# Optimization experiments

Measured on AMD Instinct MI355X. Metric: run time of the kernel, lower is better.

Reference implementation:

```python
import jax, jax.numpy as jnp
import numpy as np

NUM_MEMORIES = 4096
HIDDEN_DIM = 64
TEMPERATURE = 0.5
SHRINK_THRES = 0.0025
EPS = 1e-12


def _l2_normalize(v, axis=-1):
    # matches torch F.normalize: v / max(||v||_2, eps)
    n = jnp.sqrt(jnp.sum(v * v, axis=axis, keepdims=True))
    return v / jnp.maximum(n, EPS)


def _hard_shrink_relu(w, lambd):
    # relu(w - lambd) * w / (|w - lambd| + eps)
    d = w - lambd
    return jax.nn.relu(d) * w / (jnp.abs(d) + EPS)


def setup_inputs() -> dict:
    key = jax.random.key(0)
    kx, km = jax.random.split(key)
    x = jax.random.normal(kx, (16, 2048, HIDDEN_DIM), dtype=jnp.float32)
    # xavier_uniform for (num_memories, hidden_dim)
    bound = float(np.sqrt(6.0 / (NUM_MEMORIES + HIDDEN_DIM)))
    memories = jax.random.uniform(km, (NUM_MEMORIES, HIDDEN_DIM), dtype=jnp.float32,
                                  minval=-bound, maxval=bound)
    return {"x": x, "memories": memories}


def reference(x, memories):
    # cosine similarity addressing
    x_n = _l2_normalize(x, axis=-1)                      # [B,S,D]
    m_n = _l2_normalize(memories, axis=-1)               # [M,D]
    logits = jnp.einsum('bsd,md->bsm', x_n, m_n)         # [B,S,M]
    weight = jax.nn.softmax(logits / TEMPERATURE, axis=-1)
    # hard-shrink sparsification + L1 renormalization
    weight = _hard_shrink_relu(weight, SHRINK_THRES)
    l1 = jnp.sum(jnp.abs(weight), axis=-1, keepdims=True)
    weight = weight / jnp.maximum(l1, EPS)
    read = jnp.einsum('bsm,md->bsd', weight, memories)   # [B,S,D]
    return read, weight
```

## Files before the change

kernel.cpp:

```cpp
#include <hip/hip_runtime.h>
#include <hip/hip_bf16.h>


#define NM 4096
#define HD 64
#define NROWS 32768

typedef short bf16x8 __attribute__((ext_vector_type(8)));
typedef float f32x4  __attribute__((ext_vector_type(4)));

__global__ __launch_bounds__(256) void prep_rows(const float* __restrict__ src,
                                                 ushort* __restrict__ dst,
                                                 float scale) {
    const int wave = threadIdx.x >> 6, lane = threadIdx.x & 63;
    const long row = (long)blockIdx.x * 4 + wave;
    float v = src[row * HD + lane];
    float s = v * v;
#pragma unroll
    for (int o = 32; o; o >>= 1) s += __shfl_xor(s, o, 64);
    const float inv = scale / fmaxf(sqrtf(s), 1e-12f);
    __hip_bfloat16 h = __float2bfloat16(v * inv);
    dst[row * HD + lane] = *reinterpret_cast<ushort*>(&h);
}

__global__ __launch_bounds__(256) void prep_m_swz(const float* __restrict__ mem,
                                                  ushort* __restrict__ mbs) {
    const int wave = threadIdx.x >> 6, lane = threadIdx.x & 63;
    const int row = blockIdx.x * 4 + wave;
    float v = mem[row * HD + lane];
    float s = v * v;
#pragma unroll
    for (int o = 32; o; o >>= 1) s += __shfl_xor(s, o, 64);
    const float inv = 1.0f / fmaxf(sqrtf(s), 1e-12f);
    __hip_bfloat16 h = __float2bfloat16(v * inv);
    const int t = row >> 4, c = row & 15;
    const int k = lane;
    const int f = k >> 5, q = (k >> 3) & 3, j = k & 7;
    mbs[(long)t * 1024 + f * 512 + (q * 16 + c) * 8 + j] =
        *reinterpret_cast<ushort*>(&h);
}

__global__ __launch_bounds__(512, 4) void k_ps(const ushort* __restrict__ xb,
                                               const ushort* __restrict__ mbs,
                                               const float* __restrict__ mem,
                                               float* __restrict__ out_w,
                                               float* __restrict__ out_read) {
    const int tid = threadIdx.x;
    const int wv = tid >> 6, lane = tid & 63;
    const int m0 = blockIdx.x * 16;

    __shared__ float sS[4][16];
    __shared__ float sL[4][16];
    __shared__ uint  sD[4];
    __shared__ float sred[4][16][64];

    const float4 z4 = make_float4(0.0f, 0.0f, 0.0f, 0.0f);

    if (wv >= 4) {
        const int sw = wv - 4;
        float4* base = (float4*)(out_w + (long)m0 * NM);
#pragma unroll 8
        for (int it = 0; it < 64; it++)
            base[it * 256 + sw * 64 + lane] = z4;
        if (sw == 0) {
            float4* rb = (float4*)(out_read + (long)m0 * HD);
#pragma unroll
            for (int it = 0; it < 4; it++) rb[it * 64 + lane] = z4;
        }
        __syncthreads();
        __syncthreads();
        const uint anyd = sD[0] | sD[1] | sD[2] | sD[3];
        if (anyd) {
            __syncthreads();
            __syncthreads();
        }
        return;
    }

    const int q = lane >> 4, c = lane & 15;
    const int nbase = wv * 1024;
    const bf16x8 a0 = *(const bf16x8*)(xb + (long)(m0 + c) * HD + q * 8);
    const bf16x8 a1 = *(const bf16x8*)(xb + (long)(m0 + c) * HD + q * 8 + 32);
    const ushort* mstrip = mbs + (long)(wv * 64) * 1024;

    float tmax8[8];
    float sm[4] = {0.0f, 0.0f, 0.0f, 0.0f};
    for (int g = 0; g < 8; g++) {
        float tm = -1e30f;
#pragma unroll 4
        for (int ii = 0; ii < 8; ii++) {
            const int i = g * 8 + ii;
            const ushort* mc = mstrip + (long)i * 1024 + lane * 8;
            const bf16x8 b0 = *(const bf16x8*)(mc);
            const bf16x8 b1 = *(const bf16x8*)(mc + 512);
            f32x4 t = {0.0f, 0.0f, 0.0f, 0.0f};
            t = __builtin_amdgcn_mfma_f32_16x16x32_bf16(a0, b0, t, 0, 0, 0);
            t = __builtin_amdgcn_mfma_f32_16x16x32_bf16(a1, b1, t, 0, 0, 0);
            tm = fmaxf(tm, fmaxf(fmaxf(t[0], t[1]), fmaxf(t[2], t[3])));
#pragma unroll
            for (int r = 0; r < 4; r++) sm[r] += __expf(t[r]);
        }
        tmax8[g] = tm;
    }
#pragma unroll
    for (int o = 1; o < 16; o <<= 1)
#pragma unroll
        for (int r = 0; r < 4; r++) sm[r] += __shfl_xor(sm[r], o, 64);
    if (c == 0)
#pragma unroll
        for (int r = 0; r < 4; r++) sS[wv][q * 4 + r] = sm[r];
    __syncthreads();
    float rS[4], tmin = 1e30f;
#pragma unroll
    for (int r = 0; r < 4; r++) {
        const float S = sS[0][q * 4 + r] + sS[1][q * 4 + r] +
                        sS[2][q * 4 + r] + sS[3][q * 4 + r];
        rS[r] = 1.0f / S;
        const float tau = __logf(0.0025f * S) - 1e-3f;
        tmin = fminf(tmin, tau);
    }
    uint dmask = 0;
#pragma unroll
    for (int g = 0; g < 8; g++)
        if (__ballot(tmax8[g] > tmin)) dmask |= 1u << g;
    if (lane == 0) sD[wv] = dmask;
    __syncthreads();
    const uint anyd = sD[0] | sD[1] | sD[2] | sD[3];

    if (!anyd) return;

    float l1[4] = {0.0f, 0.0f, 0.0f, 0.0f};
    for (int g = 0; g < 8; g++) {
        if (!((dmask >> g) & 1u)) continue;
        for (int ii = 0; ii < 8; ii++) {
            const int i = g * 8 + ii;
            const ushort* mc = mstrip + (long)i * 1024 + lane * 8;
            const bf16x8 b0 = *(const bf16x8*)(mc);
            const bf16x8 b1 = *(const bf16x8*)(mc + 512);
            f32x4 t = {0.0f, 0.0f, 0.0f, 0.0f};
            t = __builtin_amdgcn_mfma_f32_16x16x32_bf16(a0, b0, t, 0, 0, 0);
            t = __builtin_amdgcn_mfma_f32_16x16x32_bf16(a1, b1, t, 0, 0, 0);
#pragma unroll
            for (int r = 0; r < 4; r++) {
                float w = __expf(t[r]) * rS[r];
                float d = w - 0.0025f;
                l1[r] += __fdividef(fmaxf(d, 0.0f) * w, fabsf(d) + 1e-12f);
            }
        }
    }
#pragma unroll
    for (int o = 1; o < 16; o <<= 1)
#pragma unroll
        for (int r = 0; r < 4; r++) l1[r] += __shfl_xor(l1[r], o, 64);
    if (c == 0)
#pragma unroll
        for (int r = 0; r < 4; r++) sL[wv][q * 4 + r] = l1[r];
    __syncthreads();
    float rL[4];
#pragma unroll
    for (int r = 0; r < 4; r++)
        rL[r] = 1.0f / fmaxf(sL[0][q * 4 + r] + sL[1][q * 4 + r] +
                             sL[2][q * 4 + r] + sL[3][q * 4 + r], 1e-12f);

    float racc[16];
#pragma unroll
    for (int r = 0; r < 16; r++) racc[r] = 0.0f;
    float* wbase = out_w + (long)(m0 + q * 4) * NM + c;
    for (int i = 0; i < 64; i++) {
        const int n0 = nbase + i * 16;
        const ushort* mc = mstrip + (long)i * 1024 + lane * 8;
        const bf16x8 b0 = *(const bf16x8*)(mc);
        const bf16x8 b1 = *(const bf16x8*)(mc + 512);
        f32x4 t = {0.0f, 0.0f, 0.0f, 0.0f};
        t = __builtin_amdgcn_mfma_f32_16x16x32_bf16(a0, b0, t, 0, 0, 0);
        t = __builtin_amdgcn_mfma_f32_16x16x32_bf16(a1, b1, t, 0, 0, 0);
        float wf[4];
#pragma unroll
        for (int r = 0; r < 4; r++) {
            float w  = __expf(t[r]) * rS[r];
            float d  = w - 0.0025f;
            float sh = __fdividef(fmaxf(d, 0.0f) * w, fabsf(d) + 1e-12f);
            wf[r] = sh * rL[r];
            wbase[(long)r * NM + n0] = wf[r];
        }
        const bool nz = (wf[0] != 0.0f) | (wf[1] != 0.0f) |
                        (wf[2] != 0.0f) | (wf[3] != 0.0f);
        unsigned long long mask = __ballot(nz);
        while (mask) {
            const int j = __ffsll((long long)mask) - 1;
            mask &= (mask - 1);
            const int qj = j >> 4, cj = j & 15;
            float b0v = __shfl(wf[0], j, 64), b1v = __shfl(wf[1], j, 64);
            float b2v = __shfl(wf[2], j, 64), b3v = __shfl(wf[3], j, 64);
            const float mv = mem[(long)(n0 + cj) * HD + lane];
            switch (qj) {
                case 0: racc[0]  += b0v * mv; racc[1]  += b1v * mv;
                        racc[2]  += b2v * mv; racc[3]  += b3v * mv; break;
                case 1: racc[4]  += b0v * mv; racc[5]  += b1v * mv;
                        racc[6]  += b2v * mv; racc[7]  += b3v * mv; break;
                case 2: racc[8]  += b0v * mv; racc[9]  += b1v * mv;
                        racc[10] += b2v * mv; racc[11] += b3v * mv; break;
                default: racc[12] += b0v * mv; racc[13] += b1v * mv;
                         racc[14] += b2v * mv; racc[15] += b3v * mv; break;
            }
        }
    }

#pragma unroll
    for (int r = 0; r < 16; r++) sred[wv][r][lane] = racc[r];
    __syncthreads();
#pragma unroll
    for (int rr = 0; rr < 4; rr++) {
        const int row = wv * 4 + rr;
        const float v = sred[0][row][lane] + sred[1][row][lane] +
                        sred[2][row][lane] + sred[3][row][lane];
        out_read[(long)(m0 + row) * HD + lane] = v;
    }
}

extern "C" void kernel_launch(void* const* d_in, const int* in_sizes, int n_in,
                              void* d_out, int out_size, void* d_ws, size_t ws_size,
                              hipStream_t stream) {
    const float* x   = (const float*)d_in[0];
    const float* mem = (const float*)d_in[1];
    ushort* xb       = (ushort*)d_ws;
    ushort* mbs      = xb + (long)NROWS * HD;
    float* out_read  = (float*)d_out;
    float* out_w     = out_read + (long)NROWS * HD;

    prep_rows<<<NROWS / 4, 256, 0, stream>>>(x, xb, 2.0f);
    prep_m_swz<<<NM / 4, 256, 0, stream>>>(mem, mbs);
    k_ps<<<NROWS / 16, 512, 0, stream>>>(xb, mbs, mem, out_w, out_read);
}
```

Measured before the change: 538.8 us.

## Process 64 rows per block to reuse memory-tile loads across row groups

Each block now handles 64 query rows in four 16-row groups, so every loaded bf16 memory tile feeds four MFMA pairs instead of one. The final write pass now visits only the tile groups flagged by the threshold mask and relies on the zeroing waves for the rest. The read output is reduced across waves with global atomicAdd instead of a shared-memory reduction. In exchange, the grid has a quarter as many blocks, each wave holds more registers for its per-row state, and atomic contention on the read rows is added.

```diff
diff --git a/kernel.cpp b/kernel.cpp
--- a/kernel.cpp
+++ b/kernel.cpp
@@ -5,6 +5,8 @@
 #define NM 4096
 #define HD 64
 #define NROWS 32768
+#define RPB 64
+#define NBLK (NROWS / RPB)
 
 typedef short bf16x8 __attribute__((ext_vector_type(8)));
 typedef float f32x4  __attribute__((ext_vector_type(4)));
@@ -40,19 +42,18 @@
         *reinterpret_cast<ushort*>(&h);
 }
 
-__global__ __launch_bounds__(512, 4) void k_ps(const ushort* __restrict__ xb,
-                                               const ushort* __restrict__ mbs,
-                                               const float* __restrict__ mem,
-                                               float* __restrict__ out_w,
-                                               float* __restrict__ out_read) {
+__global__ __launch_bounds__(512, 4) void k_ps64(const ushort* __restrict__ xb,
+                                                 const ushort* __restrict__ mbs,
+                                                 const float* __restrict__ mem,
+                                                 float* __restrict__ out_w,
+                                                 float* __restrict__ out_read) {
     const int tid = threadIdx.x;
     const int wv = tid >> 6, lane = tid & 63;
-    const int m0 = blockIdx.x * 16;
-
-    __shared__ float sS[4][16];
-    __shared__ float sL[4][16];
+    const int m0 = blockIdx.x * RPB;
+
+    __shared__ float sS[4][RPB];
+    __shared__ float sL[4][RPB];
     __shared__ uint  sD[4];
-    __shared__ float sred[4][16][64];
 
     const float4 z4 = make_float4(0.0f, 0.0f, 0.0f, 0.0f);
 
@@ -60,64 +61,68 @@
         const int sw = wv - 4;
         float4* base = (float4*)(out_w + (long)m0 * NM);
 #pragma unroll 8
-        for (int it = 0; it < 64; it++)
+        for (int it = 0; it < 256; it++)
             base[it * 256 + sw * 64 + lane] = z4;
-        if (sw == 0) {
-            float4* rb = (float4*)(out_read + (long)m0 * HD);
-#pragma unroll
-            for (int it = 0; it < 4; it++) rb[it * 64 + lane] = z4;
-        }
+        float4* rb = (float4*)(out_read + (long)m0 * HD);
+#pragma unroll
+        for (int it = 0; it < 4; it++)
+            rb[(sw * 4 + it) * 64 + lane] = z4;
         __syncthreads();
         __syncthreads();
-        const uint anyd = sD[0] | sD[1] | sD[2] | sD[3];
-        if (anyd) {
-            __syncthreads();
-            __syncthreads();
-        }
+        if (sD[0] | sD[1] | sD[2] | sD[3]) __syncthreads();
         return;
     }
 
     const int q = lane >> 4, c = lane & 15;
-    const int nbase = wv * 1024;
-    const bf16x8 a0 = *(const bf16x8*)(xb + (long)(m0 + c) * HD + q * 8);
-    const bf16x8 a1 = *(const bf16x8*)(xb + (long)(m0 + c) * HD + q * 8 + 32);
+    bf16x8 a0[4], a1[4];
+#pragma unroll
+    for (int rg = 0; rg < 4; rg++) {
+        const ushort* ap = xb + (long)(m0 + rg * 16 + c) * HD + q * 8;
+        a0[rg] = *(const bf16x8*)(ap);
+        a1[rg] = *(const bf16x8*)(ap + 32);
+    }
     const ushort* mstrip = mbs + (long)(wv * 64) * 1024;
 
+    float sm[16];
+#pragma unroll
+    for (int k = 0; k < 16; k++) sm[k] = 0.0f;
     float tmax8[8];
-    float sm[4] = {0.0f, 0.0f, 0.0f, 0.0f};
     for (int g = 0; g < 8; g++) {
         float tm = -1e30f;
-#pragma unroll 4
+#pragma unroll 2
         for (int ii = 0; ii < 8; ii++) {
             const int i = g * 8 + ii;
             const ushort* mc = mstrip + (long)i * 1024 + lane * 8;
             const bf16x8 b0 = *(const bf16x8*)(mc);
             const bf16x8 b1 = *(const bf16x8*)(mc + 512);
-            f32x4 t = {0.0f, 0.0f, 0.0f, 0.0f};
-            t = __builtin_amdgcn_mfma_f32_16x16x32_bf16(a0, b0, t, 0, 0, 0);
-            t = __builtin_amdgcn_mfma_f32_16x16x32_bf16(a1, b1, t, 0, 0, 0);
-            tm = fmaxf(tm, fmaxf(fmaxf(t[0], t[1]), fmaxf(t[2], t[3])));
-#pragma unroll
-            for (int r = 0; r < 4; r++) sm[r] += __expf(t[r]);
+#pragma unroll
+            for (int rg = 0; rg < 4; rg++) {
+                f32x4 t = {0.0f, 0.0f, 0.0f, 0.0f};
+                t = __builtin_amdgcn_mfma_f32_16x16x32_bf16(a0[rg], b0, t, 0, 0, 0);
+                t = __builtin_amdgcn_mfma_f32_16x16x32_bf16(a1[rg], b1, t, 0, 0, 0);
+                tm = fmaxf(tm, fmaxf(fmaxf(t[0], t[1]), fmaxf(t[2], t[3])));
+#pragma unroll
+                for (int r = 0; r < 4; r++) sm[rg * 4 + r] += __expf(t[r]);
+            }
         }
         tmax8[g] = tm;
     }
 #pragma unroll
     for (int o = 1; o < 16; o <<= 1)
 #pragma unroll
-        for (int r = 0; r < 4; r++) sm[r] += __shfl_xor(sm[r], o, 64);
+        for (int k = 0; k < 16; k++) sm[k] += __shfl_xor(sm[k], o, 64);
     if (c == 0)
 #pragma unroll
-        for (int r = 0; r < 4; r++) sS[wv][q * 4 + r] = sm[r];
+        for (int k = 0; k < 16; k++)
+            sS[wv][(k >> 2) * 16 + q * 4 + (k & 3)] = sm[k];
     __syncthreads();
-    float rS[4], tmin = 1e30f;
-#pragma unroll
-    for (int r = 0; r < 4; r++) {
-        const float S = sS[0][q * 4 + r] + sS[1][q * 4 + r] +
-                        sS[2][q * 4 + r] + sS[3][q * 4 + r];
-        rS[r] = 1.0f / S;
-        const float tau = __logf(0.0025f * S) - 1e-3f;
-        tmin = fminf(tmin, tau);
+    float rS[16], tmin = 1e30f;
+#pragma unroll
+    for (int k = 0; k < 16; k++) {
+        const int row = (k >> 2) * 16 + q * 4 + (k & 3);
+        const float S = sS[0][row] + sS[1][row] + sS[2][row] + sS[3][row];
+        rS[k] = 1.0f / S;
+        tmin = fminf(tmin, __logf(0.0025f * S) - 1e-3f);
     }
     uint dmask = 0;
 #pragma unroll
@@ -125,11 +130,12 @@
         if (__ballot(tmax8[g] > tmin)) dmask |= 1u << g;
     if (lane == 0) sD[wv] = dmask;
     __syncthreads();
-    const uint anyd = sD[0] | sD[1] | sD[2] | sD[3];
-
-    if (!anyd) return;
-
-    float l1[4] = {0.0f, 0.0f, 0.0f, 0.0f};
+    if (!(sD[0] | sD[1] | sD[2] | sD[3]))
+        return;
+
+    float l1[16];
+#pragma unroll
+    for (int k = 0; k < 16; k++) l1[k] = 0.0f;
     for (int g = 0; g < 8; g++) {
         if (!((dmask >> g) & 1u)) continue;
         for (int ii = 0; ii < 8; ii++) {
@@ -137,84 +143,94 @@
             const ushort* mc = mstrip + (long)i * 1024 + lane * 8;
             const bf16x8 b0 = *(const bf16x8*)(mc);
             const bf16x8 b1 = *(const bf16x8*)(mc + 512);
-            f32x4 t = {0.0f, 0.0f, 0.0f, 0.0f};
-            t = __builtin_amdgcn_mfma_f32_16x16x32_bf16(a0, b0, t, 0, 0, 0);
-            t = __builtin_amdgcn_mfma_f32_16x16x32_bf16(a1, b1, t, 0, 0, 0);
-#pragma unroll
-            for (int r = 0; r < 4; r++) {
-                float w = __expf(t[r]) * rS[r];
-                float d = w - 0.0025f;
-                l1[r] += __fdividef(fmaxf(d, 0.0f) * w, fabsf(d) + 1e-12f);
+#pragma unroll
+            for (int rg = 0; rg < 4; rg++) {
+                f32x4 t = {0.0f, 0.0f, 0.0f, 0.0f};
+                t = __builtin_amdgcn_mfma_f32_16x16x32_bf16(a0[rg], b0, t, 0, 0, 0);
+                t = __builtin_amdgcn_mfma_f32_16x16x32_bf16(a1[rg], b1, t, 0, 0, 0);
+#pragma unroll
+                for (int r = 0; r < 4; r++) {
+                    float w = __expf(t[r]) * rS[rg * 4 + r];
+                    float d = w - 0.0025f;
+                    l1[rg * 4 + r] +=
+                        __fdividef(fmaxf(d, 0.0f) * w, fabsf(d) + 1e-12f);
+                }
             }
         }
     }
 #pragma unroll
     for (int o = 1; o < 16; o <<= 1)
 #pragma unroll
-        for (int r = 0; r < 4; r++) l1[r] += __shfl_xor(l1[r], o, 64);
+        for (int k = 0; k < 16; k++) l1[k] += __shfl_xor(l1[k], o, 64);
     if (c == 0)
 #pragma unroll
-        for (int r = 0; r < 4; r++) sL[wv][q * 4 + r] = l1[r];
+        for (int k = 0; k < 16; k++)
+            sL[wv][(k >> 2) * 16 + q * 4 + (k & 3)] = l1[k];
     __syncthreads();
-    float rL[4];
-#pragma unroll
-    for (int r = 0; r < 4; r++)
-        rL[r] = 1.0f / fmaxf(sL[0][q * 4 + r] + sL[1][q * 4 + r] +
-                             sL[2][q * 4 + r] + sL[3][q * 4 + r], 1e-12f);
-
-    float racc[16];
-#pragma unroll
-    for (int r = 0; r < 16; r++) racc[r] = 0.0f;
-    float* wbase = out_w + (long)(m0 + q * 4) * NM + c;
-    for (int i = 0; i < 64; i++) {
-        const int n0 = nbase + i * 16;
-        const ushort* mc = mstrip + (long)i * 1024 + lane * 8;
-        const bf16x8 b0 = *(const bf16x8*)(mc);
-        const bf16x8 b1 = *(const bf16x8*)(mc + 512);
-        f32x4 t = {0.0f, 0.0f, 0.0f, 0.0f};
-        t = __builtin_amdgcn_mfma_f32_16x16x32_bf16(a0, b0, t, 0, 0, 0);
-        t = __builtin_amdgcn_mfma_f32_16x16x32_bf16(a1, b1, t, 0, 0, 0);
-        float wf[4];
-#pragma unroll
-        for (int r = 0; r < 4; r++) {
-            float w  = __expf(t[r]) * rS[r];
-            float d  = w - 0.0025f;
-            float sh = __fdividef(fmaxf(d, 0.0f) * w, fabsf(d) + 1e-12f);
-            wf[r] = sh * rL[r];
-            wbase[(long)r * NM + n0] = wf[r];
-        }
-        const bool nz = (wf[0] != 0.0f) | (wf[1] != 0.0f) |
-                        (wf[2] != 0.0f) | (wf[3] != 0.0f);
-        unsigned long long mask = __ballot(nz);
-        while (mask) {
-            const int j = __ffsll((long long)mask) - 1;
-            mask &= (mask - 1);
-            const int qj = j >> 4, cj = j & 15;
-            float b0v = __shfl(wf[0], j, 64), b1v = __shfl(wf[1], j, 64);
-            float b2v = __shfl(wf[2], j, 64), b3v = __shfl(wf[3], j, 64);
-            const float mv = mem[(long)(n0 + cj) * HD + lane];
-            switch (qj) {
-                case 0: racc[0]  += b0v * mv; racc[1]  += b1v * mv;
-                        racc[2]  += b2v * mv; racc[3]  += b3v * mv; break;
-                case 1: racc[4]  += b0v * mv; racc[5]  += b1v * mv;
-                        racc[6]  += b2v * mv; racc[7]  += b3v * mv; break;
-                case 2: racc[8]  += b0v * mv; racc[9]  += b1v * mv;
-                        racc[10] += b2v * mv; racc[11] += b3v * mv; break;
-                default: racc[12] += b0v * mv; racc[13] += b1v * mv;
-                         racc[14] += b2v * mv; racc[15] += b3v * mv; break;
+    float rL[16];
+#pragma unroll
+    for (int k = 0; k < 16; k++) {
+        const int row = (k >> 2) * 16 + q * 4 + (k & 3);
+        rL[k] = 1.0f / fmaxf(sL[0][row] + sL[1][row] + sL[2][row] + sL[3][row],
+                             1e-12f);
+    }
+
+    for (int rg = 0; rg < 4; rg++) {
+        float racc[16];
+#pragma unroll
+        for (int k = 0; k < 16; k++) racc[k] = 0.0f;
+        bool anyr = false;
+        float* wbase = out_w + (long)(m0 + rg * 16 + q * 4) * NM + c;
+        for (int g = 0; g < 8; g++) {
+            if (!((dmask >> g) & 1u)) continue;
+            for (int ii = 0; ii < 8; ii++) {
+                const int i = g * 8 + ii;
+                const int n0 = wv * 1024 + i * 16;
+                const ushort* mc = mstrip + (long)i * 1024 + lane * 8;
+                const bf16x8 b0 = *(const bf16x8*)(mc);
+                const bf16x8 b1 = *(const bf16x8*)(mc + 512);
+                f32x4 t = {0.0f, 0.0f, 0.0f, 0.0f};
+                t = __builtin_amdgcn_mfma_f32_16x16x32_bf16(a0[rg], b0, t, 0, 0, 0);
+                t = __builtin_amdgcn_mfma_f32_16x16x32_bf16(a1[rg], b1, t, 0, 0, 0);
+                float wf[4];
+#pragma unroll
+                for (int r = 0; r < 4; r++) {
+                    float w  = __expf(t[r]) * rS[rg * 4 + r];
+                    float d  = w - 0.0025f;
+                    float sh = __fdividef(fmaxf(d, 0.0f) * w, fabsf(d) + 1e-12f);
+                    wf[r] = sh * rL[rg * 4 + r];
+                    wbase[(long)r * NM + n0] = wf[r];
+                }
+                const bool nz = (wf[0] != 0.0f) | (wf[1] != 0.0f) |
+                                (wf[2] != 0.0f) | (wf[3] != 0.0f);
+                unsigned long long mask = __ballot(nz);
+                if (mask) anyr = true;
+                while (mask) {
+                    const int j = __ffsll((long long)mask) - 1;
+                    mask &= (mask - 1);
+                    const int qj = j >> 4, cj = j & 15;
+                    float b0v = __shfl(wf[0], j, 64), b1v = __shfl(wf[1], j, 64);
+                    float b2v = __shfl(wf[2], j, 64), b3v = __shfl(wf[3], j, 64);
+                    const float mv = mem[(long)(n0 + cj) * HD + lane];
+                    switch (qj) {
+                        case 0: racc[0]  += b0v * mv; racc[1]  += b1v * mv;
+                                racc[2]  += b2v * mv; racc[3]  += b3v * mv; break;
+                        case 1: racc[4]  += b0v * mv; racc[5]  += b1v * mv;
+                                racc[6]  += b2v * mv; racc[7]  += b3v * mv; break;
+                        case 2: racc[8]  += b0v * mv; racc[9]  += b1v * mv;
+                                racc[10] += b2v * mv; racc[11] += b3v * mv; break;
+                        default: racc[12] += b0v * mv; racc[13] += b1v * mv;
+                                 racc[14] += b2v * mv; racc[15] += b3v * mv; break;
+                    }
+                }
             }
         }
-    }
-
-#pragma unroll
-    for (int r = 0; r < 16; r++) sred[wv][r][lane] = racc[r];
-    __syncthreads();
-#pragma unroll
-    for (int rr = 0; rr < 4; rr++) {
-        const int row = wv * 4 + rr;
-        const float v = sred[0][row][lane] + sred[1][row][lane] +
-                        sred[2][row][lane] + sred[3][row][lane];
-        out_read[(long)(m0 + row) * HD + lane] = v;
+        if (anyr) {
+#pragma unroll
+            for (int k = 0; k < 16; k++)
+                atomicAdd(out_read + (long)(m0 + rg * 16 + k) * HD + lane,
+                          racc[k]);
+        }
     }
 }
 
@@ -230,5 +246,5 @@
 
     prep_rows<<<NROWS / 4, 256, 0, stream>>>(x, xb, 2.0f);
     prep_m_swz<<<NM / 4, 256, 0, stream>>>(mem, mbs);
-    k_ps<<<NROWS / 16, 512, 0, stream>>>(xb, mbs, mem, out_w, out_read);
-}
+    k_ps64<<<NBLK, 512, 0, stream>>>(xb, mbs, mem, out_w, out_read);
+}
```

Result: slower. 558.5 us (+3.7%).
